# Kernel tuning notes

Hardware: AMD Instinct MI355X
Metric: run time of the kernel (lower is better)

Reference implementation:

```python
import jax, jax.numpy as jnp
import numpy as np

K = 5
K2 = K * K  # 25
SLOPE = 0.01  # torch leaky_relu default


def _unfold(x, k):
    # torch.nn.Unfold(k) on reflect-padded x: channel order c-major, then kh, kw
    b, c, h, w = x.shape
    p = k // 2
    xp = jnp.pad(x, ((0, 0), (0, 0), (p, p), (p, p)), mode='reflect')
    cols = jnp.stack([xp[:, :, i:i + h, j:j + w] for i in range(k) for j in range(k)], axis=2)
    return cols.reshape(b, c * k * k, h * w)  # (b, 3*k^2, h*w)


def _lin(x, W, b):
    # torch Linear: W is (out, in)
    return x @ W.T + b


def _lrelu(x):
    return jnp.where(x >= 0, x, SLOPE * x)


def setup_inputs() -> dict:
    key = jax.random.key(0)
    ks = iter(jax.random.split(key, 64))
    d = {}
    d['x'] = jax.random.uniform(next(ks), (4, 3, 384, 384), dtype=jnp.float32)

    def mk(name, out_f, in_f):
        d['W_' + name] = jax.random.normal(next(ks), (out_f, in_f), jnp.float32) * (1.0 / np.sqrt(in_f))
        d['b_' + name] = jax.random.normal(next(ks), (out_f,), jnp.float32) * 0.01

    mk('input', 2 * K2, 3 * K2)
    mk('h1', 3 * K2, 2 * K2)
    mk('h2', 3 * K2, 3 * K2)
    mk('h3', 2 * K2, 2 * K2)
    mk('h4', 5 * K2, 2 * K2)
    mk('h5', 2 * K2, 5 * K2)
    mk('out', 3, 2 * K2)
    # encoder(3*k^2): in -> 3*in -> in -> 3
    mk('e1', 9 * K2, 3 * K2); mk('e2', 3 * K2, 9 * K2); mk('e3', 3, 3 * K2)
    # encoder(2*k^2)
    mk('f1', 6 * K2, 2 * K2); mk('f2', 2 * K2, 6 * K2); mk('f3', 3, 2 * K2)
    # decoder(2*k^2): 3 -> out -> 3*out -> out
    mk('d1', 2 * K2, 3); mk('d2', 6 * K2, 2 * K2); mk('d3', 2 * K2, 6 * K2)
    return d


def reference(x,
              W_input, b_input, W_h1, b_h1, W_h2, b_h2, W_h3, b_h3,
              W_h4, b_h4, W_h5, b_h5, W_out, b_out,
              W_e1, b_e1, W_e2, b_e2, W_e3, b_e3,
              W_f1, b_f1, W_f2, b_f2, W_f3, b_f3,
              W_d1, b_d1, W_d2, b_d2, W_d3, b_d3):
    b, c, h, w = x.shape
    sw = jnp.transpose(_unfold(x, K), (0, 2, 1))  # (b, h*w, 3*k^2)
    x1 = _lin(sw, W_input, b_input)
    x2 = _lrelu(_lin(x1, W_h1, b_h1))
    x3 = jnp.tanh(_lin(x2, W_h2, b_h2))
    x3_enc = _lin(_lin(_lin(x3, W_e1, b_e1), W_e2, b_e2), W_e3, b_e3)
    enc2_x1 = _lin(_lin(_lin(x1, W_f1, b_f1), W_f2, b_f2), W_f3, b_f3)
    x4 = _lrelu(x3_enc + enc2_x1)
    x4_dec = _lin(_lin(_lin(_lin(x4, W_d1, b_d1), W_d2, b_d2), W_d3, b_d3), W_h3, b_h3)
    x5 = jnp.tanh(_lin(x4_dec, W_h4, b_h4))
    x6 = _lin(x5, W_h5, b_h5) - x1
    x7 = _lrelu(_lin(x6, W_out, b_out))  # (b, h*w, 3)
    return jnp.transpose(x7, (0, 2, 1)).reshape(b, c, h, w)
```

## Files before the change

### kernel.cpp

```cpp
#include <hip/hip_runtime.h>


#define IW 384
#define HW (384 * 384)
#define NPIX (4 * HW)
#define MTILE 192
#define NBLK (NPIX / MTILE)

#define TANH_SCALE 2.8853900817779268f

typedef _Float16 half8 __attribute__((ext_vector_type(8)));
typedef _Float16 h2v __attribute__((ext_vector_type(2)));
typedef __fp16 fp16x2 __attribute__((ext_vector_type(2)));
typedef __attribute__((ext_vector_type(4))) float f32x4;
typedef __attribute__((ext_vector_type(4))) unsigned int uint4_;

#define MFMAH(A, B, C) __builtin_amdgcn_mfma_f32_16x16x32_f16((A), (B), (C), 0, 0, 0)

#define BA   0
#define B1   64
#define B2   144
#define BEF  224
#define BD   240
#define B4   304
#define B5   432
#define BOUT 496
#define BIAS_TOT 512

#define W_A0   0
#define W_A1   2048
#define W_A2   4096
#define W_H1A  6144
#define W_H1B  8704
#define W_H2A  11264
#define W_H2B  13824
#define W_H2C  16384
#define W_EF   18944
#define W_D    24064
#define W_H4C0 28160
#define W_H5C0 30208
#define W_OUT  44544
#define W_NI   45568
#define W_TOT  47616

#define STG_BE  24320
#define STG_BF  24336

__device__ __forceinline__ float lrelu(float v) { return fmaxf(v, 0.01f * v); }

#if __has_builtin(__builtin_amdgcn_exp2f)
#define EXP2F __builtin_amdgcn_exp2f
#else
#define EXP2F __builtin_exp2f
#endif

__device__ __forceinline__ float tanh_fast(float v) {
    float e = EXP2F(v);
    return __builtin_fmaf(-2.0f, __builtin_amdgcn_rcpf(e + 1.0f), 1.0f);
}

__device__ __forceinline__ unsigned short f2h_bits(float v) {
    union { _Float16 h; unsigned short s; } u; u.h = (_Float16)v; return u.s;
}
__device__ __forceinline__ float h2f_bits(unsigned short s) {
    union { _Float16 h; unsigned short s; } u; u.s = s; return (float)u.h;
}
__device__ __forceinline__ unsigned packh2(float a, float b) {
    union { fp16x2 h; unsigned u; } u;
    u.h = __builtin_amdgcn_cvt_pkrtz(a, b);
    return u.u;
}

__device__ __forceinline__ unsigned lrelu_pkh(unsigned x) {
    union { unsigned u; h2v h; } a, b, r;
    a.u = x;
    b.h = a.h * (h2v)((_Float16)0.01f);
    r.h = __builtin_elementwise_max(a.h, b.h);
    return r.u;
}

__device__ __forceinline__ void stage(float* dst, const float* __restrict__ src,
                                      int n, int tid) {
    int n4 = n >> 2;
    float4* d = (float4*)dst;
    const float4* s = (const float4*)src;
#pragma unroll 4
    for (int i = tid; i < n4; i += 256) d[i] = s[i];
    for (int i = (n4 << 2) + tid; i < n; i += 256) dst[i] = src[i];
}

__global__ __launch_bounds__(256) void setup_all(
    const float* __restrict__ W_input, const float* __restrict__ b_input,
    const float* __restrict__ W_h1,  const float* __restrict__ b_h1,
    const float* __restrict__ W_h2,  const float* __restrict__ b_h2,
    const float* __restrict__ W_h3,  const float* __restrict__ b_h3,
    const float* __restrict__ W_h4,  const float* __restrict__ b_h4,
    const float* __restrict__ W_h5,  const float* __restrict__ b_h5,
    const float* __restrict__ W_out, const float* __restrict__ b_out,
    const float* __restrict__ W_e1,  const float* __restrict__ b_e1,
    const float* __restrict__ W_e2,  const float* __restrict__ b_e2,
    const float* __restrict__ W_e3,  const float* __restrict__ b_e3,
    const float* __restrict__ W_f1,  const float* __restrict__ b_f1,
    const float* __restrict__ W_f2,  const float* __restrict__ b_f2,
    const float* __restrict__ W_f3,  const float* __restrict__ b_f3,
    const float* __restrict__ W_d1,  const float* __restrict__ b_d1,
    const float* __restrict__ W_d2,  const float* __restrict__ b_d2,
    const float* __restrict__ W_d3,  const float* __restrict__ b_d3,
    float* __restrict__ ws)
{
    const int tid = threadIdx.x;
    const int NT = 256;
    short* wimg = (short*)(ws + BIAS_TOT);

    if (blockIdx.x < 71) {
        const int soff[17] = {W_A0,W_A1,W_A2, W_H1A,W_H1B, W_H2A,W_H2B,W_H2C,
                              W_H4C0,W_H5C0, W_H4C0+4096,W_H5C0+4096,
                              W_H4C0+8192,W_H5C0+8192, W_H4C0+12288,W_H5C0+12288,
                              W_OUT};
        const int slay[17] = {0,0,0, 1,1, 2,2,2, 6,7, 6,7, 6,7, 6,7, 8};
        const int sNT[17]  = {4,4,4, 5,5, 5,5,5, 2,4, 2,4, 2,4, 2,4, 1};
        const int sKTS[17] = {1,1,1, 1,1, 1,1,1, 2,1, 2,1, 2,1, 2,1, 2};
        const int snb[17]  = {0,0,0, 0,0, 0,0,0, 0,0, 32,0, 64,0, 96,0, 0};
        const int skb[17]  = {0,32,64, 0,32, 0,32,64, 0,0, 0,32, 0,64, 0,96, 0};

        int seg = 0, local = blockIdx.x;
        while (seg < 16 && local >= sNT[seg] * sKTS[seg]) { local -= sNT[seg] * sKTS[seg]; seg++; }
        const int kts = sKTS[seg];
        const int kt = local % kts, nt = local / kts;
        const int lay = slay[seg];
        short* dst = wimg + soff[seg] + local * 512;

#pragma unroll
        for (int t = 0; t < 2; t++) {
            int idx = tid + t * 256;
            int j = idx & 7, lane = idx >> 3;
            int slot = (lay == 0) ? ((lane >> 4) * 8 + j)
                                  : (4 * (lane >> 4) + (j & 3) + 16 * (j >> 2));
            int n = snb[seg] + nt * 16 + (lane & 15);
            int k = skb[seg] + kt * 32 + slot;
            float v = 0.0f;
            switch (lay) {
                case 0: if (n < 50  && k < 75)  v = W_input[n * 75 + k]; break;
                case 1: if (n < 75  && k < 50)  v = W_h1[n * 50 + k]; break;
                case 2: if (n < 75  && k < 75)  v = W_h2[n * 75 + k] * TANH_SCALE; break;
                case 6: if (n < 125 && k < 50)  v = W_h4[n * 50 + k] * TANH_SCALE; break;
                case 7: if (n < 50  && k < 125) v = W_h5[n * 125 + k]; break;
                case 8: if (n < 3   && k < 50)  v = W_out[n * 50 + k]; break;
            }
            dst[idx] = (short)f2h_bits(v);
        }
        return;
    }

    if (blockIdx.x == 74) {
        for (int i = tid; i < BIAS_TOT; i += NT) {
            if (i >= BD && i < B4) continue;
            float v = 0.0f;
            if (i < B1)        { int o = i - BA;   if (o < 50)  v = b_input[o]; }
            else if (i < B2)   { int o = i - B1;   if (o < 75)  v = b_h1[o]; }
            else if (i < BEF)  { int o = i - B2;   if (o < 75)  v = b_h2[o] * TANH_SCALE; }
            else if (i < BD)   { v = 0.0f; }
            else if (i < B5)   { int o = i - B4;   if (o < 125) v = b_h4[o] * TANH_SCALE; }
            else if (i < BOUT) { int o = i - B5;   if (o < 50)  v = b_h5[o]; }
            else               { int o = i - BOUT; if (o < 3)   v = b_out[o]; }
            ws[i] = v;
        }
        for (int i = tid; i < 2048; i += NT) {
            int j = i & 7, lane = (i >> 3) & 63, nt = i >> 9;
            int n = nt * 16 + (lane & 15);
            int k = (nt >> 1) * 32 + 4 * (lane >> 4) + (j & 3) + 16 * (j >> 2);
            wimg[W_NI + i] = (short)f2h_bits(k == n ? -1.0f : 0.0f);
        }
        return;
    }

    __shared__ __align__(16) float A[17500];
    __shared__ float B[675];
    __shared__ float C[256];
    __shared__ float Dd[256];
    __shared__ float Es[256];
    __shared__ float S[232];

    if (blockIdx.x == 71) {
        stage(A, W_e2, 16875, tid);
        for (int i = tid; i < 225; i += NT) { Es[i] = W_e3[i]; C[i] = b_e1[i]; }
        __syncthreads();
        for (int o = tid; o < 675; o += NT) {
            int r = o / 225, c = o % 225;
            float s0 = 0.f, s1 = 0.f, s2 = 0.f;
#pragma unroll
            for (int t = 0; t < 75; t += 3) {
                s0 += Es[r * 75 + t]     * A[t * 225 + c];
                s1 += Es[r * 75 + t + 1] * A[(t + 1) * 225 + c];
                s2 += Es[r * 75 + t + 2] * A[(t + 2) * 225 + c];
            }
            B[o] = s0 + s1 + s2;
        }
        for (int o = tid; o < 75; o += NT) {
            float s0 = 0.f, s1 = 0.f, s2 = 0.f;
#pragma unroll
            for (int t = 0; t < 225; t += 3) {
                s0 += A[o * 225 + t]     * C[t];
                s1 += A[o * 225 + t + 1] * C[t + 1];
                s2 += A[o * 225 + t + 2] * C[t + 2];
            }
            Dd[o] = b_e2[o] + s0 + s1 + s2;
        }
        __syncthreads();
        stage(A, W_e1, 16875, tid);
        __syncthreads();
        for (int o = tid; o < 225; o += NT) {
            int r = o / 75, c = o % 75;
            float s0 = 0.f, s1 = 0.f, s2 = 0.f;
#pragma unroll
            for (int t = 0; t < 225; t += 3) {
                s0 += B[r * 225 + t]     * A[t * 75 + c];
                s1 += B[r * 225 + t + 1] * A[(t + 1) * 75 + c];
                s2 += B[r * 225 + t + 2] * A[(t + 2) * 75 + c];
            }
            S[o] = s0 + s1 + s2;
        }
        for (int o = tid; o < 16; o += NT) {
            float s = 0.0f;
            if (o < 3) {
                s = b_e3[o];
                for (int t = 0; t < 75; t++) s += Es[o * 75 + t] * Dd[t];
            }
            ws[STG_BE + o] = s;
        }
        __syncthreads();
        for (int i = tid; i < 3072; i += NT) {
            int j = i & 7, lane = (i >> 3) & 63, frag = i >> 9, pl = frag & 1, kt = frag >> 1;
            int n = lane & 15;
            int k = kt * 32 + 4 * (lane >> 4) + (j & 3) + 16 * (j >> 2);
            float v = (n < 3 && k < 75) ? S[n * 75 + k] : 0.0f;
            float hi = h2f_bits(f2h_bits(v));
            wimg[W_EF + i] = (short)(pl ? f2h_bits(v - hi) : f2h_bits(v));
        }
    } else if (blockIdx.x == 72) {
        stage(A,        W_f2, 7500, tid);
        stage(A + 7500, W_f1, 7500, tid);
        for (int i = tid; i < 150; i += NT) { Es[i] = W_f3[i]; C[i] = b_f1[i]; }
        __syncthreads();
        for (int o = tid; o < 450; o += NT) {
            int r = o / 150, c = o % 150;
            float s0 = 0.f, s1 = 0.f;
#pragma unroll
            for (int t = 0; t < 50; t += 2) {
                s0 += Es[r * 50 + t]     * A[t * 150 + c];
                s1 += Es[r * 50 + t + 1] * A[(t + 1) * 150 + c];
            }
            B[o] = s0 + s1;
        }
        for (int o = tid; o < 50; o += NT) {
            float s0 = 0.f, s1 = 0.f;
#pragma unroll
            for (int t = 0; t < 150; t += 2) {
                s0 += A[o * 150 + t]     * C[t];
                s1 += A[o * 150 + t + 1] * C[t + 1];
            }
            Dd[o] = b_f2[o] + s0 + s1;
        }
        __syncthreads();
        for (int o = tid; o < 150; o += NT) {
            int r = o / 50, c = o % 50;
            float s0 = 0.f, s1 = 0.f;
#pragma unroll
            for (int t = 0; t < 150; t += 2) {
                s0 += B[r * 150 + t]     * A[7500 + t * 50 + c];
                s1 += B[r * 150 + t + 1] * A[7500 + (t + 1) * 50 + c];
            }
            S[o] = s0 + s1;
        }
        for (int o = tid; o < 16; o += NT) {
            float s = 0.0f;
            if (o < 3) {
                s = b_f3[o];
                for (int t = 0; t < 50; t++) s += Es[o * 50 + t] * Dd[t];
            }
            ws[STG_BF + o] = s;
        }
        __syncthreads();
        for (int i = tid; i < 2048; i += NT) {
            int j = i & 7, lane = (i >> 3) & 63, frag = i >> 9, pl = frag & 1, kt = frag >> 1;
            int n = lane & 15;
            int k = kt * 32 + 4 * (lane >> 4) + (j & 3) + 16 * (j >> 2);
            float v = (n < 3 && k < 50) ? S[n * 50 + k] : 0.0f;
            float hi = h2f_bits(f2h_bits(v));
            wimg[W_EF + 3072 + i] = (short)(pl ? f2h_bits(v - hi) : f2h_bits(v));
        }
    } else {
        stage(A,         W_d2, 7500, tid);
        stage(A + 7500,  W_d3, 7500, tid);
        stage(A + 15000, W_h3, 2500, tid);
        for (int i = tid; i < 150; i += NT) Es[i] = W_d1[i];
        for (int i = tid; i < 50;  i += NT) C[i] = b_d1[i];
        __syncthreads();
        for (int o = tid; o < 450; o += NT) {
            int r = o / 3, c = o % 3;
            float s0 = 0.f, s1 = 0.f;
#pragma unroll
            for (int t = 0; t < 50; t += 2) {
                s0 += A[r * 50 + t]     * Es[t * 3 + c];
                s1 += A[r * 50 + t + 1] * Es[(t + 1) * 3 + c];
            }
            B[o] = s0 + s1;
        }
        for (int o = tid; o < 150; o += NT) {
            float s0 = 0.f, s1 = 0.f;
#pragma unroll
            for (int t = 0; t < 50; t += 2) {
                s0 += A[o * 50 + t]     * C[t];
                s1 += A[o * 50 + t + 1] * C[t + 1];
            }
            Dd[o] = b_d2[o] + s0 + s1;
        }
        __syncthreads();
        for (int o = tid; o < 150; o += NT) {
            int r = o / 3, c = o % 3;
            float s0 = 0.f, s1 = 0.f;
#pragma unroll
            for (int t = 0; t < 150; t += 2) {
                s0 += A[7500 + r * 150 + t]     * B[t * 3 + c];
                s1 += A[7500 + r * 150 + t + 1] * B[(t + 1) * 3 + c];
            }
            Es[o] = s0 + s1;
        }
        for (int o = tid; o < 50; o += NT) {
            float s0 = 0.f, s1 = 0.f;
#pragma unroll
            for (int t = 0; t < 150; t += 2) {
                s0 += A[7500 + o * 150 + t]     * Dd[t];
                s1 += A[7500 + o * 150 + t + 1] * Dd[t + 1];
            }
            C[o] = b_d3[o] + s0 + s1;
        }
        __syncthreads();
        for (int o = tid; o < 150; o += NT) {
            int r = o / 3, c = o % 3;
            float s0 = 0.f, s1 = 0.f;
#pragma unroll
            for (int t = 0; t < 50; t += 2) {
                s0 += A[15000 + r * 50 + t]     * Es[t * 3 + c];
                s1 += A[15000 + r * 50 + t + 1] * Es[(t + 1) * 3 + c];
            }
            S[o] = s0 + s1;
        }
        for (int o = tid; o < 64; o += NT) {
            float v = 0.0f;
            if (o < 50) {
                float s0 = 0.f, s1 = 0.f;
#pragma unroll
                for (int t = 0; t < 50; t += 2) {
                    s0 += A[15000 + o * 50 + t]     * C[t];
                    s1 += A[15000 + o * 50 + t + 1] * C[t + 1];
                }
                v = b_h3[o] + s0 + s1;
            }
            ws[BD + o] = v;
        }
        __syncthreads();
        for (int i = tid; i < 4096; i += NT) {
            int j = i & 7, lane = (i >> 3) & 63, frag = i >> 9, pl = frag & 1, nt = frag >> 1;
            int n = nt * 16 + (lane & 15);
            int k = 4 * (lane >> 4) + (j & 3) + 16 * (j >> 2);
            float v = (n < 50 && k < 3) ? S[n * 3 + k] : 0.0f;
            float hi = h2f_bits(f2h_bits(v));
            wimg[W_D + i] = (short)(pl ? f2h_bits(v - hi) : f2h_bits(v));
        }
    }
}

__device__ __forceinline__ half8 gfragH(const short* __restrict__ wl, int off) {
    return *(const half8*)(wl + off);
}

__device__ __forceinline__ half8 packB(f32x4 lo, f32x4 hi) {
    union { unsigned u32[4]; half8 v; } u;
    u.u32[0] = packh2(lo[0], lo[1]);
    u.u32[1] = packh2(lo[2], lo[3]);
    u.u32[2] = packh2(hi[0], hi[1]);
    u.u32[3] = packh2(hi[2], hi[3]);
    return u.v;
}
__device__ __forceinline__ half8 packB1(f32x4 lo) {
    union { unsigned u32[4]; half8 v; } u;
    u.u32[0] = packh2(lo[0], lo[1]);
    u.u32[1] = packh2(lo[2], lo[3]);
    u.u32[2] = 0u; u.u32[3] = 0u;
    return u.v;
}
__device__ __forceinline__ half8 packB_lr(f32x4 lo, f32x4 hi) {
    union { unsigned u32[4]; half8 v; } u;
    u.u32[0] = lrelu_pkh(packh2(lo[0], lo[1]));
    u.u32[1] = lrelu_pkh(packh2(lo[2], lo[3]));
    u.u32[2] = lrelu_pkh(packh2(hi[0], hi[1]));
    u.u32[3] = lrelu_pkh(packh2(hi[2], hi[3]));
    return u.v;
}
__device__ __forceinline__ half8 packB1_lr(f32x4 lo) {
    union { unsigned u32[4]; half8 v; } u;
    u.u32[0] = lrelu_pkh(packh2(lo[0], lo[1]));
    u.u32[1] = lrelu_pkh(packh2(lo[2], lo[3]));
    u.u32[2] = 0u; u.u32[3] = 0u;
    return u.v;
}

__device__ __forceinline__ void st16(unsigned int* p, half8 v) {
    union { half8 h; uint4_ u; } c; c.h = v;
    *(uint4_*)p = c.u;
}
__device__ __forceinline__ half8 ld16(const unsigned int* p) {
    union { half8 h; uint4_ u; } c; c.u = *(const uint4_*)p;
    return c.h;
}

__device__ __forceinline__ f32x4 lrelu4(f32x4 v) {
    v[0] = lrelu(v[0]); v[1] = lrelu(v[1]); v[2] = lrelu(v[2]); v[3] = lrelu(v[3]);
    return v;
}
__device__ __forceinline__ f32x4 tanh4(f32x4 v) {
    v[0] = tanh_fast(v[0]); v[1] = tanh_fast(v[1]);
    v[2] = tanh_fast(v[2]); v[3] = tanh_fast(v[3]);
    return v;
}

__global__ __launch_bounds__(256, 4) void fused_mfma(
    const float* __restrict__ xin,
    const float* __restrict__ ws,
    float* __restrict__ out)
{
    __shared__ float patch[2940];
    __shared__ int stab[96];
    __shared__ unsigned int x1buf[6144];

    const int tid = threadIdx.x;
    const int wv = tid >> 6;
    const int lane = tid & 63;
    const int qd = lane >> 4;
    const int mcol = lane & 15;
    const short* __restrict__ wl = (const short*)(ws + BIAS_TOT) + lane * 8;

    const int g0 = blockIdx.x * MTILE;
    const int bb = g0 / HW;
    const int p0 = g0 - bb * HW;
    const int yb = p0 / IW;
    const int xblk = p0 - yb * IW;
    const float* __restrict__ xb = xin + bb * 3 * HW;

    unsigned int* xpark = x1buf + wv * 1536 + lane * 4;

    {
        int tyr[5];
#pragma unroll
        for (int r = 0; r < 5; r++) {
            int ty = yb + r - 2; ty = ty < 0 ? -ty : ty; ty = (766 - ty) < ty ? 766 - ty : ty;
            tyr[r] = ty * IW;
        }
        if (tid < 196) {
            int tx = xblk - 2 + tid; tx = tx < 0 ? -tx : tx; tx = (766 - tx) < tx ? 766 - tx : tx;
#pragma unroll
            for (int cr = 0; cr < 15; cr++) {
                const int c = cr / 5, r = cr % 5;
                patch[cr * 196 + tid] = xb[c * HW + tyr[r] + tx];
            }
        }
    }
    if (tid < 96) {
        int v = 0;
        if (tid < 75) {
            int c = tid / 25, rem = tid - 25 * c;
            int rr = rem / 5, ss = rem - 5 * rr;
            v = (c * 5 + rr) * 196 + ss;
        }
        stab[tid] = v;
    }
    __syncthreads();

    half8 swf[3][3];
    {
        int st[3][8];
#pragma unroll
        for (int kt = 0; kt < 3; kt++)
#pragma unroll
            for (int j = 0; j < 8; j++)
                st[kt][j] = stab[kt * 32 + qd * 8 + j];
#pragma unroll
        for (int pt = 0; pt < 3; pt++) {
            const int xloc = wv * 48 + pt * 16 + mcol;
#pragma unroll
            for (int kt = 0; kt < 3; kt++) {
                union { unsigned u32[4]; half8 v; } u;
#pragma unroll
                for (int jj = 0; jj < 8; jj += 2) {
                    float v0 = patch[st[kt][jj]     + xloc];
                    float v1 = patch[st[kt][jj + 1] + xloc];
                    u.u32[jj >> 1] = packh2(v0, v1);
                }
                swf[kt][pt] = u.v;
            }
        }
    }

    half8 x1f[2][3];
#pragma unroll
    for (int g = 0; g < 2; g++) {
        const short* wlg = wl;
        asm volatile("" : "+v"(wlg));
        f32x4 acc[2][3];
#pragma unroll
        for (int m = 0; m < 2; m++) {
            f32x4 b = *(const f32x4*)(ws + BA + (2 * g + m) * 16 + qd * 4);
            acc[m][0] = b; acc[m][1] = b; acc[m][2] = b;
        }
#pragma unroll
        for (int kt = 0; kt < 3; kt++)
#pragma unroll
            for (int m = 0; m < 2; m++) {
                half8 w = gfragH(wlg, W_A0 + kt * 2048 + (2 * g + m) * 512);
#pragma unroll
                for (int pt = 0; pt < 3; pt++)
                    acc[m][pt] = MFMAH(w, swf[kt][pt], acc[m][pt]);
            }
#pragma unroll
        for (int pt = 0; pt < 3; pt++) {
            x1f[g][pt] = packB(acc[0][pt], acc[1][pt]);
            st16(xpark + g * 768 + pt * 256, x1f[g][pt]);
        }
    }

    half8 x2f[3][3];
#pragma unroll
    for (int g = 0; g < 2; g++) {
        const short* wlg = wl;
        asm volatile("" : "+v"(wlg));
        f32x4 acc[2][3];
#pragma unroll
        for (int m = 0; m < 2; m++) {
            f32x4 b = *(const f32x4*)(ws + B1 + (2 * g + m) * 16 + qd * 4);
            acc[m][0] = b; acc[m][1] = b; acc[m][2] = b;
        }
#pragma unroll
        for (int kt = 0; kt < 2; kt++)
#pragma unroll
            for (int m = 0; m < 2; m++) {
                half8 w = gfragH(wlg, W_H1A + kt * 2560 + (2 * g + m) * 512);
#pragma unroll
                for (int pt = 0; pt < 3; pt++)
                    acc[m][pt] = MFMAH(w, x1f[kt][pt], acc[m][pt]);
            }
#pragma unroll
        for (int pt = 0; pt < 3; pt++)
            x2f[g][pt] = packB_lr(acc[0][pt], acc[1][pt]);
    }
    {
        const short* wlg = wl;
        asm volatile("" : "+v"(wlg));
        f32x4 acc[3];
        {
            f32x4 b = *(const f32x4*)(ws + B1 + 4 * 16 + qd * 4);
            acc[0] = b; acc[1] = b; acc[2] = b;
        }
#pragma unroll
        for (int kt = 0; kt < 2; kt++) {
            half8 w = gfragH(wlg, W_H1A + kt * 2560 + 4 * 512);
#pragma unroll
            for (int pt = 0; pt < 3; pt++)
                acc[pt] = MFMAH(w, x1f[kt][pt], acc[pt]);
        }
#pragma unroll
        for (int pt = 0; pt < 3; pt++)
            x2f[2][pt] = packB1_lr(acc[pt]);
    }

    f32x4 accEF[3];
    {
        f32x4 be = *(const f32x4*)(ws + STG_BE + qd * 4);
        f32x4 bf = *(const f32x4*)(ws + STG_BF + qd * 4);
        f32x4 b = be + bf;
        accEF[0] = b; accEF[1] = b; accEF[2] = b;
    }
#pragma unroll
    for (int g = 0; g < 2; g++) {
        const short* wlg = wl;
        asm volatile("" : "+v"(wlg));
        f32x4 acc[2][3];
#pragma unroll
        for (int m = 0; m < 2; m++) {
            f32x4 b = *(const f32x4*)(ws + B2 + (2 * g + m) * 16 + qd * 4);
            acc[m][0] = b; acc[m][1] = b; acc[m][2] = b;
        }
#pragma unroll
        for (int kt = 0; kt < 3; kt++)
#pragma unroll
            for (int m = 0; m < 2; m++) {
                half8 w = gfragH(wlg, W_H2A + kt * 2560 + (2 * g + m) * 512);
#pragma unroll
                for (int pt = 0; pt < 3; pt++)
                    acc[m][pt] = MFMAH(w, x2f[kt][pt], acc[m][pt]);
            }
        half8 wh = gfragH(wlg, W_EF + g * 1024);
        half8 wo = gfragH(wlg, W_EF + g * 1024 + 512);
#pragma unroll
        for (int pt = 0; pt < 3; pt++) {
            half8 t = packB(tanh4(acc[0][pt]), tanh4(acc[1][pt]));
            accEF[pt] = MFMAH(wh, t, accEF[pt]);
            accEF[pt] = MFMAH(wo, t, accEF[pt]);
        }
    }
    {
        const short* wlg = wl;
        asm volatile("" : "+v"(wlg));
        f32x4 acc[3];
        {
            f32x4 b = *(const f32x4*)(ws + B2 + 4 * 16 + qd * 4);
            acc[0] = b; acc[1] = b; acc[2] = b;
        }
#pragma unroll
        for (int kt = 0; kt < 3; kt++) {
            half8 w = gfragH(wlg, W_H2A + kt * 2560 + 4 * 512);
#pragma unroll
            for (int pt = 0; pt < 3; pt++)
                acc[pt] = MFMAH(w, x2f[kt][pt], acc[pt]);
        }
        half8 wh = gfragH(wlg, W_EF + 2 * 1024);
        half8 wo = gfragH(wlg, W_EF + 2 * 1024 + 512);
#pragma unroll
        for (int pt = 0; pt < 3; pt++) {
            half8 t = packB1(tanh4(acc[pt]));
            accEF[pt] = MFMAH(wh, t, accEF[pt]);
            accEF[pt] = MFMAH(wo, t, accEF[pt]);
        }
    }
    half8 x1r[2][3];
#pragma unroll
    for (int kt = 0; kt < 2; kt++)
#pragma unroll
        for (int pt = 0; pt < 3; pt++)
            x1r[kt][pt] = ld16(xpark + kt * 768 + pt * 256);
#pragma unroll
    for (int kt = 0; kt < 2; kt++) {
        half8 wh = gfragH(wl, W_EF + 3072 + kt * 1024);
        half8 wo = gfragH(wl, W_EF + 3072 + kt * 1024 + 512);
#pragma unroll
        for (int pt = 0; pt < 3; pt++) {
            accEF[pt] = MFMAH(wh, x1r[kt][pt], accEF[pt]);
            accEF[pt] = MFMAH(wo, x1r[kt][pt], accEF[pt]);
        }
    }
    half8 x4f[3];
#pragma unroll
    for (int pt = 0; pt < 3; pt++)
        x4f[pt] = packB1_lr(accEF[pt]);

    f32x4 x6a[4][3];
#pragma unroll
    for (int mt = 0; mt < 4; mt++) {
        f32x4 b = *(const f32x4*)(ws + B5 + mt * 16 + qd * 4);
        half8 nI = gfragH(wl, W_NI + mt * 512);
#pragma unroll
        for (int pt = 0; pt < 3; pt++)
            x6a[mt][pt] = MFMAH(nI, x1r[mt >> 1][pt], b);
    }

#pragma unroll
    for (int h = 0; h < 2; h++) {
        f32x4 accD[2][3];
#pragma unroll
        for (int m2 = 0; m2 < 2; m2++) {
            f32x4 b = *(const f32x4*)(ws + BD + (h * 2 + m2) * 16 + qd * 4);
            accD[m2][0] = b; accD[m2][1] = b; accD[m2][2] = b;
        }
#pragma unroll
        for (int m2 = 0; m2 < 2; m2++) {
            int mt = h * 2 + m2;
            half8 wh = gfragH(wl, W_D + mt * 1024);
            half8 wo = gfragH(wl, W_D + mt * 1024 + 512);
#pragma unroll
            for (int pt = 0; pt < 3; pt++) {
                accD[m2][pt] = MFMAH(wh, x4f[pt], accD[m2][pt]);
                accD[m2][pt] = MFMAH(wo, x4f[pt], accD[m2][pt]);
            }
        }
#pragma unroll
        for (int pt = 0; pt < 3; pt++)
            st16(xpark + h * 768 + pt * 256, packB(accD[0][pt], accD[1][pt]));
    }

#pragma unroll
    for (int c = 0; c < 4; c++) {
        const unsigned int* xr = xpark;
        asm volatile("" : "+v"(xr));
        half8 xd[2][3];
#pragma unroll
        for (int kt = 0; kt < 2; kt++)
#pragma unroll
            for (int pt = 0; pt < 3; pt++)
                xd[kt][pt] = ld16(xr + kt * 768 + pt * 256);
        f32x4 acc5[2][3];
#pragma unroll
        for (int mt2 = 0; mt2 < 2; mt2++) {
            f32x4 b = *(const f32x4*)(ws + B4 + c * 32 + mt2 * 16 + qd * 4);
            acc5[mt2][0] = b; acc5[mt2][1] = b; acc5[mt2][2] = b;
        }
#pragma unroll
        for (int kt = 0; kt < 2; kt++)
#pragma unroll
            for (int mt2 = 0; mt2 < 2; mt2++) {
                half8 w = gfragH(wl, W_H4C0 + c * 4096 + (mt2 * 2 + kt) * 512);
#pragma unroll
                for (int pt = 0; pt < 3; pt++)
                    acc5[mt2][pt] = MFMAH(w, xd[kt][pt], acc5[mt2][pt]);
            }
        half8 chf[3];
#pragma unroll
        for (int pt = 0; pt < 3; pt++)
            chf[pt] = packB(tanh4(acc5[0][pt]), tanh4(acc5[1][pt]));
#pragma unroll
        for (int mt = 0; mt < 4; mt++) {
            half8 w = gfragH(wl, W_H5C0 + c * 4096 + mt * 512);
#pragma unroll
            for (int pt = 0; pt < 3; pt++)
                x6a[mt][pt] = MFMAH(w, chf[pt], x6a[mt][pt]);
        }
    }

    f32x4 accO[3];
    {
        f32x4 b = *(const f32x4*)(ws + BOUT + qd * 4);
        accO[0] = b; accO[1] = b; accO[2] = b;
    }
#pragma unroll
    for (int kt = 0; kt < 2; kt++) {
        half8 w = gfragH(wl, W_OUT + kt * 512);
#pragma unroll
        for (int pt = 0; pt < 3; pt++) {
            half8 x6f = packB(x6a[2 * kt][pt], x6a[2 * kt + 1][pt]);
            accO[pt] = MFMAH(w, x6f, accO[pt]);
        }
    }
    if (qd == 0) {
#pragma unroll
        for (int pt = 0; pt < 3; pt++) {
            int p = p0 + wv * 48 + pt * 16 + mcol;
#pragma unroll
            for (int r = 0; r < 3; r++)
                out[(bb * 3 + r) * HW + p] = lrelu(accO[pt][r]);
        }
    }
}

extern "C" void kernel_launch(void* const* d_in, const int* in_sizes, int n_in,
                              void* d_out, int out_size, void* d_ws, size_t ws_size,
                              hipStream_t stream)
{
    const float* xin = (const float*)d_in[0];
    float* ws = (float*)d_ws;

    setup_all<<<75, 256, 0, stream>>>(
        (const float*)d_in[1],  (const float*)d_in[2],
        (const float*)d_in[3],  (const float*)d_in[4],
        (const float*)d_in[5],  (const float*)d_in[6],
        (const float*)d_in[7],  (const float*)d_in[8],
        (const float*)d_in[9],  (const float*)d_in[10],
        (const float*)d_in[11], (const float*)d_in[12],
        (const float*)d_in[13], (const float*)d_in[14],
        (const float*)d_in[15], (const float*)d_in[16],
        (const float*)d_in[17], (const float*)d_in[18],
        (const float*)d_in[19], (const float*)d_in[20],
        (const float*)d_in[21], (const float*)d_in[22],
        (const float*)d_in[23], (const float*)d_in[24],
        (const float*)d_in[25], (const float*)d_in[26],
        (const float*)d_in[27], (const float*)d_in[28],
        (const float*)d_in[29], (const float*)d_in[30],
        (const float*)d_in[31], (const float*)d_in[32],
        ws);

    fused_mfma<<<NBLK, 256, 0, stream>>>(xin, ws, (float*)d_out);
}
```

Before: 203.8 us.

## Restructure tail layers to process one pixel tile at a time in registers

Reorders the decoder, h4/h5 chunk loop and output layer so each of the three pixel subtiles runs the full chain before moving to the next. The intermediate decoder output is no longer parked in LDS and reloaded; it stays in registers as packed halves. This shrinks live accumulator state (x6a from 4x3 to 4) to cut register pressure and LDS traffic. In exchange, weight fragments are reloaded three times, once per subtile, and MFMA chains have less independent work to hide latency.

```diff
diff --git a/kernel.cpp b/kernel.cpp
--- a/kernel.cpp
+++ b/kernel.cpp
@@ -415,10 +415,6 @@
     return c.h;
 }
 
-__device__ __forceinline__ f32x4 lrelu4(f32x4 v) {
-    v[0] = lrelu(v[0]); v[1] = lrelu(v[1]); v[2] = lrelu(v[2]); v[3] = lrelu(v[3]);
-    return v;
-}
 __device__ __forceinline__ f32x4 tanh4(f32x4 v) {
     v[0] = tanh_fast(v[0]); v[1] = tanh_fast(v[1]);
     v[2] = tanh_fast(v[2]); v[3] = tanh_fast(v[3]);
@@ -653,99 +649,50 @@
     for (int pt = 0; pt < 3; pt++)
         x4f[pt] = packB1_lr(accEF[pt]);
 
-    f32x4 x6a[4][3];
-#pragma unroll
-    for (int mt = 0; mt < 4; mt++) {
-        f32x4 b = *(const f32x4*)(ws + B5 + mt * 16 + qd * 4);
-        half8 nI = gfragH(wl, W_NI + mt * 512);
-#pragma unroll
-        for (int pt = 0; pt < 3; pt++)
-            x6a[mt][pt] = MFMAH(nI, x1r[mt >> 1][pt], b);
-    }
-
-#pragma unroll
-    for (int h = 0; h < 2; h++) {
-        f32x4 accD[2][3];
-#pragma unroll
-        for (int m2 = 0; m2 < 2; m2++) {
-            f32x4 b = *(const f32x4*)(ws + BD + (h * 2 + m2) * 16 + qd * 4);
-            accD[m2][0] = b; accD[m2][1] = b; accD[m2][2] = b;
-        }
-#pragma unroll
-        for (int m2 = 0; m2 < 2; m2++) {
-            int mt = h * 2 + m2;
-            half8 wh = gfragH(wl, W_D + mt * 1024);
-            half8 wo = gfragH(wl, W_D + mt * 1024 + 512);
-#pragma unroll
-            for (int pt = 0; pt < 3; pt++) {
-                accD[m2][pt] = MFMAH(wh, x4f[pt], accD[m2][pt]);
-                accD[m2][pt] = MFMAH(wo, x4f[pt], accD[m2][pt]);
-            }
-        }
-#pragma unroll
-        for (int pt = 0; pt < 3; pt++)
-            st16(xpark + h * 768 + pt * 256, packB(accD[0][pt], accD[1][pt]));
-    }
-
-#pragma unroll
-    for (int c = 0; c < 4; c++) {
-        const unsigned int* xr = xpark;
-        asm volatile("" : "+v"(xr));
-        half8 xd[2][3];
-#pragma unroll
-        for (int kt = 0; kt < 2; kt++)
-#pragma unroll
-            for (int pt = 0; pt < 3; pt++)
-                xd[kt][pt] = ld16(xr + kt * 768 + pt * 256);
-        f32x4 acc5[2][3];
-#pragma unroll
-        for (int mt2 = 0; mt2 < 2; mt2++) {
-            f32x4 b = *(const f32x4*)(ws + B4 + c * 32 + mt2 * 16 + qd * 4);
-            acc5[mt2][0] = b; acc5[mt2][1] = b; acc5[mt2][2] = b;
-        }
-#pragma unroll
-        for (int kt = 0; kt < 2; kt++)
-#pragma unroll
-            for (int mt2 = 0; mt2 < 2; mt2++) {
-                half8 w = gfragH(wl, W_H4C0 + c * 4096 + (mt2 * 2 + kt) * 512);
-#pragma unroll
-                for (int pt = 0; pt < 3; pt++)
-                    acc5[mt2][pt] = MFMAH(w, xd[kt][pt], acc5[mt2][pt]);
-            }
-        half8 chf[3];
-#pragma unroll
-        for (int pt = 0; pt < 3; pt++)
-            chf[pt] = packB(tanh4(acc5[0][pt]), tanh4(acc5[1][pt]));
+#pragma unroll
+    for (int pt = 0; pt < 3; pt++) {
+        const short* wlp = wl;
+        asm volatile("" : "+v"(wlp));
+        f32x4 x6a[4];
 #pragma unroll
         for (int mt = 0; mt < 4; mt++) {
-            half8 w = gfragH(wl, W_H5C0 + c * 4096 + mt * 512);
-#pragma unroll
-            for (int pt = 0; pt < 3; pt++)
-                x6a[mt][pt] = MFMAH(w, chf[pt], x6a[mt][pt]);
-        }
-    }
-
-    f32x4 accO[3];
-    {
-        f32x4 b = *(const f32x4*)(ws + BOUT + qd * 4);
-        accO[0] = b; accO[1] = b; accO[2] = b;
-    }
-#pragma unroll
-    for (int kt = 0; kt < 2; kt++) {
-        half8 w = gfragH(wl, W_OUT + kt * 512);
-#pragma unroll
-        for (int pt = 0; pt < 3; pt++) {
-            half8 x6f = packB(x6a[2 * kt][pt], x6a[2 * kt + 1][pt]);
-            accO[pt] = MFMAH(w, x6f, accO[pt]);
-        }
-    }
-    if (qd == 0) {
-#pragma unroll
-        for (int pt = 0; pt < 3; pt++) {
+            f32x4 b = *(const f32x4*)(ws + B5 + mt * 16 + qd * 4);
+            half8 nI = gfragH(wlp, W_NI + mt * 512);
+            x6a[mt] = MFMAH(nI, x1r[mt >> 1][pt], b);
+        }
+        f32x4 accD[4];
+#pragma unroll
+        for (int mt = 0; mt < 4; mt++) {
+            f32x4 b = *(const f32x4*)(ws + BD + mt * 16 + qd * 4);
+            half8 wh = gfragH(wlp, W_D + mt * 1024);
+            half8 wo = gfragH(wlp, W_D + mt * 1024 + 512);
+            accD[mt] = MFMAH(wh, x4f[pt], b);
+            accD[mt] = MFMAH(wo, x4f[pt], accD[mt]);
+        }
+        half8 xd0 = packB(accD[0], accD[1]);
+        half8 xd1 = packB(accD[2], accD[3]);
+#pragma unroll
+        for (int c = 0; c < 4; c++) {
+            f32x4 a0 = *(const f32x4*)(ws + B4 + c * 32 + qd * 4);
+            f32x4 a1 = *(const f32x4*)(ws + B4 + c * 32 + 16 + qd * 4);
+            a0 = MFMAH(gfragH(wlp, W_H4C0 + c * 4096 + 0 * 512), xd0, a0);
+            a0 = MFMAH(gfragH(wlp, W_H4C0 + c * 4096 + 1 * 512), xd1, a0);
+            a1 = MFMAH(gfragH(wlp, W_H4C0 + c * 4096 + 2 * 512), xd0, a1);
+            a1 = MFMAH(gfragH(wlp, W_H4C0 + c * 4096 + 3 * 512), xd1, a1);
+            half8 chf = packB(tanh4(a0), tanh4(a1));
+#pragma unroll
+            for (int mt = 0; mt < 4; mt++)
+                x6a[mt] = MFMAH(gfragH(wlp, W_H5C0 + c * 4096 + mt * 512),
+                                chf, x6a[mt]);
+        }
+        f32x4 accO = *(const f32x4*)(ws + BOUT + qd * 4);
+        accO = MFMAH(gfragH(wlp, W_OUT),       packB(x6a[0], x6a[1]), accO);
+        accO = MFMAH(gfragH(wlp, W_OUT + 512), packB(x6a[2], x6a[3]), accO);
+        if (qd == 0) {
             int p = p0 + wv * 48 + pt * 16 + mcol;
 #pragma unroll
             for (int r = 0; r < 3; r++)
-                out[(bb * 3 + r) * HW + p] = lrelu(accO[pt][r]);
+                out[(bb * 3 + r) * HW + p] = lrelu(accO[r]);
         }
     }
 }
```

New measurement: 232.7 us. 1.14x slower.
